# Kernel tuning notes

Measured on AMD Instinct MI355X. Metric: run time of the kernel, lower is better.

The kernel has to match this reference:

```python
import jax, jax.numpy as jnp
import numpy as np

N = 32768   # nodes
E = 131072  # directed edges
B = 8       # graphs in batch
F_IN = 1025
NEG = -1e30
EPS = 1e-5


def _lin_init(k, i, o):
    k1, k2 = jax.random.split(k)
    s = 1.0 / np.sqrt(i)
    return (jax.random.uniform(k1, (i, o), jnp.float32, -s, s),
            jax.random.uniform(k2, (o,), jnp.float32, -s, s))


def _bn_init(k, c):
    k1, k2, k3, k4 = jax.random.split(k, 4)
    gamma = jax.random.uniform(k1, (c,), jnp.float32, 0.5, 1.5)
    beta = jax.random.normal(k2, (c,), jnp.float32) * 0.1
    mean = jax.random.normal(k3, (c,), jnp.float32) * 0.1
    var = jax.random.uniform(k4, (c,), jnp.float32, 0.5, 1.5)
    return jnp.stack([gamma, beta, mean, var])  # [4, c]


def setup_inputs() -> dict:
    key = jax.random.key(0)
    ks = jax.random.split(key, 16)
    x = jax.random.normal(ks[0], (N, F_IN), jnp.float32)
    edge_index = jax.random.randint(ks[1], (2, E), 0, N, dtype=jnp.int32)
    batch = jnp.sort(jax.random.randint(ks[2], (N,), 0, B, dtype=jnp.int32))
    pool_w, pool_b = _lin_init(ks[3], 2 * F_IN, 1)
    c1_w0, _ = _lin_init(ks[4], F_IN, 512)
    c1_w1, c1_b = _lin_init(ks[5], F_IN, 512)
    c2_w0, _ = _lin_init(ks[6], 512, 512)
    c2_w1, c2_b = _lin_init(ks[7], 512, 512)
    bn1 = _bn_init(ks[8], 512)
    bn2 = _bn_init(ks[9], 512)
    bn3 = _bn_init(ks[10], 512)
    bn4 = _bn_init(ks[11], 256)
    lin1_w, lin1_b = _lin_init(ks[12], 1024, 512)
    lin2_w, lin2_b = _lin_init(ks[13], 512, 256)
    lin3_w, lin3_b = _lin_init(ks[14], 256, 4)
    return dict(x=x, edge_index=edge_index, batch=batch,
                pool_w=pool_w, pool_b=pool_b,
                c1_w0=c1_w0, c1_w1=c1_w1, c1_b=c1_b,
                c2_w0=c2_w0, c2_w1=c2_w1, c2_b=c2_b,
                bn1=bn1, bn2=bn2, bn3=bn3, bn4=bn4,
                lin1_w=lin1_w, lin1_b=lin1_b,
                lin2_w=lin2_w, lin2_b=lin2_b,
                lin3_w=lin3_w, lin3_b=lin3_b)


def _batchnorm(h, p):
    g, b, m, v = p[0], p[1], p[2], p[3]
    return (h - m) * jax.lax.rsqrt(v + EPS) * g + b


def _cheb(h, row, col, w, w0, w1, b):
    # ChebConv K=2, sym norm, lambda_max=2: out = h@W0 + (L_hat h)@W1 + b,
    # L_hat = -D^{-1/2} A D^{-1/2} (self-loops removed, diag of scaled L is 0)
    deg = jax.ops.segment_sum(w, row, num_segments=N)
    dis = jnp.where(deg > 0, 1.0 / jnp.sqrt(jnp.maximum(deg, 1e-12)), 0.0)
    nrm = -w * dis[row] * dis[col]
    tx1 = jax.ops.segment_sum(nrm[:, None] * h[row], col, num_segments=N)
    return h @ w0 + tx1 @ w1 + b


def _forward(x, edge_index, batch, pool_w, pool_b,
             c1_w0, c1_w1, c1_b, c2_w0, c2_w1, c2_b,
             bn1, bn2, bn3, bn4,
             lin1_w, lin1_b, lin2_w, lin2_b, lin3_w, lin3_b):
    u, v = edge_index[0], edge_index[1]

    # ---- EdgePooling: edge scores = softmax over dst segments, +0.5 ----
    e = (jnp.concatenate([x[u], x[v]], axis=1) @ pool_w + pool_b)[:, 0]  # [E]
    m = jax.ops.segment_max(e, v, num_segments=N)
    ex = jnp.exp(e - m[v])
    score = ex / jax.ops.segment_sum(ex, v, num_segments=N)[v] + 0.5

    # ---- greedy maximal matching in descending score order ----
    order = jnp.argsort(-score)

    def step(used, k):
        uu, vv = u[k], v[k]
        ok = jnp.logical_not(used[uu] | used[vv])
        used = used.at[uu].set(used[uu] | ok)
        used = used.at[vv].set(used[vv] | ok)
        return used, ok

    _, ok_sorted = jax.lax.scan(step, jnp.zeros((N,), bool), order)
    sel = jnp.zeros((E,), bool).at[order].set(ok_sorted)

    rep = jnp.minimum(u, v)  # cluster representative of a merged edge
    cluster = jnp.arange(N, dtype=jnp.int32)
    cluster = cluster.at[jnp.where(sel, u, N)].set(rep, mode='drop')
    cluster = cluster.at[jnp.where(sel, v, N)].set(rep, mode='drop')
    node_score = jnp.ones((N,), x.dtype).at[jnp.where(sel, rep, N)].set(score, mode='drop')
    px = jnp.zeros_like(x).at[cluster].add(x) * node_score[:, None]  # pooled node feats
    valid = cluster == jnp.arange(N, dtype=jnp.int32)  # surviving cluster rows

    # ---- coarsened edge_index, coalesced (dedup), self-loops dropped ----
    cu, cv = cluster[u], cluster[v]
    nonloop = cu != cv
    key = jnp.where(nonloop, cu * N + cv, N * N + jnp.arange(E, dtype=jnp.int32))
    o2 = jnp.argsort(key)
    sk = key[o2]
    first = jnp.concatenate([jnp.ones((1,), bool), sk[1:] != sk[:-1]])
    keep_sorted = first & (sk < N * N)
    w = jnp.zeros((E,), x.dtype).at[o2].set(keep_sorted.astype(x.dtype))

    # ---- two ChebConv + BN(eval) + ReLU ----
    h = jax.nn.relu(_batchnorm(_cheb(px, cu, cv, w, c1_w0, c1_w1, c1_b), bn1))
    h = jax.nn.relu(_batchnorm(_cheb(h, cu, cv, w, c2_w0, c2_w1, c2_b), bn2))

    # ---- global max + mean pool over valid nodes per graph ----
    hmax = jax.ops.segment_max(jnp.where(valid[:, None], h, NEG), batch, num_segments=B)
    cnt = jax.ops.segment_sum(valid.astype(h.dtype), batch, num_segments=B)
    hmean = jax.ops.segment_sum(jnp.where(valid[:, None], h, 0.0), batch,
                                num_segments=B) / jnp.maximum(cnt, 1.0)[:, None]
    g = jnp.concatenate([hmax, hmean], axis=1)  # [B, 1024]

    # ---- readout MLP (dropout off in eval) ----
    g = jax.nn.relu(_batchnorm(g @ lin1_w + lin1_b, bn3))
    g = jax.nn.relu(_batchnorm(g @ lin2_w + lin2_b, bn4))
    feature = g
    out = jax.nn.log_softmax(jax.nn.relu(g @ lin3_w + lin3_b), axis=-1)
    return out, feature


def reference(x, edge_index, batch, pool_w, pool_b,
              c1_w0, c1_w1, c1_b, c2_w0, c2_w1, c2_b,
              bn1, bn2, bn3, bn4,
              lin1_w, lin1_b, lin2_w, lin2_b, lin3_w, lin3_b):
    return _forward(x, edge_index, batch, pool_w, pool_b,
                    c1_w0, c1_w1, c1_b, c2_w0, c2_w1, c2_b,
                    bn1, bn2, bn3, bn4,
                    lin1_w, lin1_b, lin2_w, lin2_b, lin3_w, lin3_b)
```

## Files before the change

### kernel.cpp

```cpp
#include <hip/hip_runtime.h>
#include <hip/hip_bf16.h>
#include <cstdint>
#include <cmath>

typedef unsigned int u32;
typedef unsigned long long u64;
typedef float f32x4 __attribute__((ext_vector_type(4)));
typedef __bf16 bf16x8 __attribute__((ext_vector_type(8)));
typedef unsigned short us8 __attribute__((ext_vector_type(8)));
typedef unsigned short us4 __attribute__((ext_vector_type(4)));

#define NN 32768
#define NE 131072
#define FIN 1025
#define HTS 262144
#define HTM (HTS - 1)

#define WS_A_D    0ul
#define WS_B_D    262144ul
#define WS_EMAX   524288ul
#define WS_SSUM   655360ul
#define WS_EXD    917504ul
#define WS_CIN    917504ul
#define WS_KEY    1966080ul
#define WS_BEST   3014656ul
#define WS_USED   3276800ul
#define WS_CUR    3276800ul
#define WS_ACT0   3407872ul
#define WS_ACT1   3932160ul
#define WS_BTHI   0ul
#define WS_BT2    3407872ul
#define WS_HT     1966080ul
#define WS_RACC1  2097152ul
#define WS_RACC2  2113536ul
#define WS_SCORE  4456448ul
#define WS_CSRA   4456448ul
#define WS_SEL    4980736ul
#define WS_CSRC   4980736ul
#define WS_CLUST  5505024ul
#define WS_OTHER  5636096ul
#define WS_NSC    5767168ul
#define WS_CEU    5898240ul
#define WS_CEV    6422528ul
#define WS_DEG    6946816ul
#define WS_OFF    6946816ul
#define WS_DIS    7077888ul
#define WS_PXL    7077888ul
#define WS_MISC   7208960ul
#define WS_GMAX   7209216ul
#define WS_GSUM   7225600ul
#define WS_GCNT   7241984ul
#define WS_P      7242240ul
#define WS_PB     74351104ul
#define WS_H      141459968ul

__device__ __forceinline__ u32 enc_f(float f) {
    u32 b = __float_as_uint(f);
    return (b & 0x80000000u) ? ~b : (b | 0x80000000u);
}
__device__ __forceinline__ float dec_f(u32 m) {
    return (m & 0x80000000u) ? __uint_as_float(m ^ 0x80000000u) : __uint_as_float(~m);
}
__device__ __forceinline__ double wave_sum(double v) {
    #pragma unroll
    for (int off = 32; off > 0; off >>= 1) v += __shfl_down(v, off, 64);
    return v;
}
__device__ __forceinline__ unsigned short f2bf(float v) {
    u32 b = __float_as_uint(v);
    u32 r = b + 0x7FFFu + ((b >> 16) & 1u);
    return (unsigned short)(r >> 16);
}
__device__ __forceinline__ float bf2f(unsigned short h) {
    return __uint_as_float(((u32)h) << 16);
}
__device__ __forceinline__ bf16x8 ld_frag(const unsigned short* p) {
    union { us8 u; bf16x8 b; } t;
    t.u = *(const us8*)p;
    return t.b;
}
__device__ __forceinline__ void dma16(unsigned short* lds, const unsigned short* g) {
    __builtin_amdgcn_global_load_lds((const __attribute__((address_space(1))) u32*)g,
                                     (__attribute__((address_space(3))) u32*)lds, 16, 0, 0);
}

__global__ void node_dots(const float* __restrict__ x, const float* __restrict__ pw,
                          double* a_d, double* b_d,
                          u32* emax, double* ssum, u32* deg, int* misc,
                          u32* gmaxb, float* gsum, float* gcnt,
                          u64* best, u32* used, int* clus, int* other, float* nsc) {
    int gid = blockIdx.x * blockDim.x + threadIdx.x;
    if (gid < NN) {
        emax[gid] = 0u; ssum[gid] = 0.0; deg[gid] = 0u;
        best[gid] = ~0ull; used[gid] = 0u;
        clus[gid] = gid; other[gid] = -1; nsc[gid] = 1.0f;
    }
    if (gid < 4096) { gmaxb[gid] = 0u; gsum[gid] = 0.0f; }
    if (gid < 64) { misc[gid] = (gid == 1) ? NE : 0; gcnt[gid] = 0.0f; }

    int wave = gid >> 6;
    int lane = threadIdx.x & 63;
    if (wave >= NN) return;
    const float* xr = x + (size_t)wave * FIN;
    double s0 = 0.0, s1 = 0.0;
    for (int f = lane; f < FIN; f += 64) {
        double xv = (double)xr[f];
        s0 += xv * (double)pw[f];
        s1 += xv * (double)pw[FIN + f];
    }
    s0 = wave_sum(s0); s1 = wave_sum(s1);
    if (lane == 0) { a_d[wave] = s0; b_d[wave] = s1; }
}

__global__ void edge_p1(const int* __restrict__ ei, const double* __restrict__ a_d,
                        const double* __restrict__ b_d, const float* __restrict__ pb,
                        double* e_d, u32* emax) {
    int k = blockIdx.x * 256 + threadIdx.x;
    if (k >= NE) return;
    int u = ei[k], v = ei[NE + k];
    double e = a_d[u] + b_d[v] + (double)pb[0];
    e_d[k] = e;
    atomicMax(&emax[v], enc_f((float)e));
}
__global__ void edge_p2(const int* __restrict__ ei, double* e_d,
                        const u32* __restrict__ emax, double* ssum) {
    int k = blockIdx.x * 256 + threadIdx.x;
    if (k >= NE) return;
    int v = ei[NE + k];
    float mf = dec_f(emax[v]);
    double ex = exp(e_d[k] - (double)mf);
    e_d[k] = ex;
    unsafeAtomicAdd(&ssum[v], ex);
}
__global__ void edge_p3(const int* __restrict__ ei, const double* __restrict__ e_d,
                        const double* __restrict__ ssum, float* score, u64* key,
                        int* sel, int* act0, u64* best) {
    int k = blockIdx.x * 256 + threadIdx.x;
    if (k >= NE) return;
    int u = ei[k], v = ei[NE + k];
    float sc = (float)(e_d[k] / ssum[v] + 0.5);
    score[k] = sc;
    u32 m = enc_f(sc);
    u64 kk = ((u64)(m ^ 0xFFFFFFFFu) << 32) | (u32)k;
    key[k] = kk;
    sel[k] = 0;
    act0[k] = k;
    atomicMin(&best[u], kk);
    atomicMin(&best[v], kk);
}

__global__ void mk_sel(const u64* __restrict__ key, const int* __restrict__ ei,
                       const int* __restrict__ act, const int* __restrict__ cntp,
                       int* ncntp, const u64* __restrict__ best,
                       u32* used, int* sel) {
    int cnt = cntp[0];
    int stride = gridDim.x * blockDim.x;
    int gid = blockIdx.x * blockDim.x + threadIdx.x;
    if (gid == 0) ncntp[0] = 0;
    for (int i = gid; i < cnt; i += stride) {
        int e = act[i];
        u64 k = key[e];
        int a = ei[e], b = ei[NE + e];
        if (best[a] == k && best[b] == k) { sel[e] = 1; used[a] = 1u; used[b] = 1u; }
    }
}
__global__ void mk_compact(const int* __restrict__ ei, const int* __restrict__ act,
                           const int* __restrict__ cntp, int* nxt, int* ncntp,
                           u64* best, const u32* __restrict__ used) {
    int cnt = cntp[0];
    int stride = gridDim.x * blockDim.x;
    for (int i = blockIdx.x * blockDim.x + threadIdx.x; i < cnt; i += stride) {
        int e = act[i];
        int a = ei[e], b = ei[NE + e];
        best[a] = ~0ull; best[b] = ~0ull;
        bool live = !(used[a] | used[b]);
        u64 mask = __ballot(live);
        if (mask) {
            int lane = threadIdx.x & 63;
            int leader = __ffsll((unsigned long long)mask) - 1;
            int base = 0;
            if (lane == leader) base = atomicAdd(ncntp, __popcll(mask));
            base = __shfl(base, leader, 64);
            if (live) nxt[base + __popcll(mask & ((1ull << lane) - 1ull))] = e;
        }
    }
}
__global__ void mk_min(const u64* __restrict__ key, const int* __restrict__ ei,
                       const int* __restrict__ act, const int* __restrict__ cntp,
                       u64* best) {
    int cnt = cntp[0];
    int stride = gridDim.x * blockDim.x;
    for (int i = blockIdx.x * blockDim.x + threadIdx.x; i < cnt; i += stride) {
        int e = act[i];
        u64 k = key[e];
        atomicMin(&best[ei[e]], k);
        atomicMin(&best[ei[NE + e]], k);
    }
}
__global__ void __launch_bounds__(1024) match_fin(
        const u64* __restrict__ key, const int* __restrict__ ei,
        int* sel, u64* best, u32* used,
        int* listA, int* listB, const int* __restrict__ cntp) {
    int tid = threadIdx.x;
    int cnt = cntp[0];
    int* cur = listA; int* nxt = listB;
    __shared__ int s_n;
    for (int round = 0; round < 4096 && cnt > 0; ++round) {
        for (int i = tid; i < cnt; i += 1024) {
            int e = cur[i]; u64 k = key[e];
            atomicMin(&best[ei[e]], k);
            atomicMin(&best[ei[NE + e]], k);
        }
        __syncthreads();
        for (int i = tid; i < cnt; i += 1024) {
            int e = cur[i]; u64 k = key[e];
            int a = ei[e], b = ei[NE + e];
            if (best[a] == k && best[b] == k) { sel[e] = 1; used[a] = 1u; used[b] = 1u; }
        }
        if (tid == 0) s_n = 0;
        __syncthreads();
        for (int i = tid; i < cnt; i += 1024) {
            int e = cur[i];
            int a = ei[e], b = ei[NE + e];
            best[a] = ~0ull; best[b] = ~0ull;
            if (!(used[a] | used[b])) {
                int idx = atomicAdd(&s_n, 1);
                nxt[idx] = e;
            }
        }
        __syncthreads();
        cnt = s_n;
        int* t = cur; cur = nxt; nxt = t;
        __syncthreads();
    }
}

__global__ void apply_sel(const int* __restrict__ ei, const int* __restrict__ sel,
                          const float* __restrict__ score,
                          int* cluster, int* other, float* nscore,
                          u32* ht, u32* cin) {
    int e = blockIdx.x * 256 + threadIdx.x;
    ht[e << 1] = 0xFFFFFFFFu;
    ht[(e << 1) + 1] = 0xFFFFFFFFu;
    if (e < NN) cin[e] = 0u;
    if (sel[e] != 1) return;
    int u = ei[e], v = ei[NE + e];
    int rep = min(u, v);
    cluster[u] = rep; cluster[v] = rep;
    if (u != v) other[rep] = u + v - rep;
    nscore[rep] = score[e];
}

__global__ void coarse_build(const int* __restrict__ ei, const int* __restrict__ cluster,
                             u32* ht, int* misc, int* ce_u, int* ce_v, u32* deg,
                             u32* cin) {
    int e = blockIdx.x * 256 + threadIdx.x;
    if (e >= NE) return;
    int cu = cluster[ei[e]], cv = cluster[ei[NE + e]];
    if (cu == cv) return;
    u32 k = (u32)cu * 32768u + (u32)cv;
    u32 h = ((k * 2654435761u) >> 12) & HTM;
    while (true) {
        u32 old = atomicCAS(&ht[h], 0xFFFFFFFFu, k);
        if (old == 0xFFFFFFFFu) {
            int idx = atomicAdd(&misc[0], 1);
            ce_u[idx] = cu; ce_v[idx] = cv;
            atomicAdd(&deg[cu], 1u);
            atomicAdd(&cin[cv], 1u);
            break;
        }
        if (old == k) break;
        h = (h + 1) & HTM;
    }
}
__global__ void dis_kernel(const u32* __restrict__ deg, float* dis,
                           float* racc1, float* racc2,
                           const int* __restrict__ clus, const int* __restrict__ batch,
                           float* gcnt) {
    int n = blockIdx.x * 256 + threadIdx.x;
    if (n >= NN) return;
    u32 d = deg[n];
    dis[n] = d ? (float)(1.0 / sqrt((double)d)) : 0.0f;
    if (n < 4096) racc1[n] = 0.0f;
    if (n < 2048) racc2[n] = 0.0f;
    bool val = (clus[n] == n);
    int bt = batch[n];
    int lane = threadIdx.x & 63;
    #pragma unroll
    for (int g = 0; g < 8; ++g) {
        u64 m = __ballot(val && bt == g);
        if (m && lane == (__ffsll((unsigned long long)m) - 1))
            unsafeAtomicAdd(&gcnt[g], (float)__popcll(m));
    }
}

__global__ void __launch_bounds__(1024) scan_kernel(const u32* __restrict__ cin,
                                                    int* off, int* cur) {
    __shared__ int part[1024];
    int t = threadIdx.x;
    int base = t << 5;
    int loc[32];
    int s = 0;
    #pragma unroll
    for (int i = 0; i < 32; ++i) { loc[i] = s; s += (int)cin[base + i]; }
    part[t] = s;
    __syncthreads();
    for (int d = 1; d < 1024; d <<= 1) {
        int v = (t >= d) ? part[t - d] : 0;
        __syncthreads();
        if (t >= d) part[t] += v;
        __syncthreads();
    }
    int pre = (t == 0) ? 0 : part[t - 1];
    #pragma unroll
    for (int i = 0; i < 32; ++i) {
        int v = pre + loc[i];
        off[base + i] = v;
        cur[base + i] = v;
    }
}
__global__ void csr_scatter(const int* __restrict__ ce_u, const int* __restrict__ ce_v,
                            const float* __restrict__ dis, const int* __restrict__ misc,
                            int* cur, int* csr_a, float* csr_c) {
    int e = blockIdx.x * 256 + threadIdx.x;
    if (e >= misc[0]) return;
    int a = ce_u[e], b = ce_v[e];
    int pos = atomicAdd(&cur[b], 1);
    csr_a[pos] = a;
    csr_c[pos] = -dis[a] * dis[b];
}

__device__ __forceinline__ size_t pk_idx(int r, int k, int KT) {
    return ((((size_t)(r >> 4) * KT + (k >> 5)) << 6) + (((k >> 3) & 3) << 4) + (r & 15)) << 3;
}

__global__ void __launch_bounds__(256) conv_all(
        const float* __restrict__ x, const int* __restrict__ clus,
        const int* __restrict__ other, const float* __restrict__ nsc,
        unsigned short* __restrict__ Abf, float* __restrict__ pxl,
        const float* __restrict__ B10, const float* __restrict__ B11,
        unsigned short* __restrict__ Bp1,
        const float* __restrict__ B20, const float* __restrict__ B21,
        unsigned short* __restrict__ Bp2) {
    int bid = blockIdx.x;
    int t = threadIdx.x;
    if (bid < 2048) {
        int tile = bid;
        int wave = t >> 6, lane = t & 63;
        int l16 = lane & 15, quad = lane >> 4;
        int row = (tile << 4) + l16;
        bool valid = (clus[row] == row);
        int o = other[row];
        float s = nsc[row];
        const float* xr = x + (size_t)row * FIN;
        const float* xo = x + (size_t)(o >= 0 ? o : row) * FIN;
        for (int kt = wave; kt < 32; kt += 4) {
            int c0 = (kt << 5) + (quad << 3);
            unsigned short h[8];
            #pragma unroll
            for (int j = 0; j < 8; ++j) {
                float v = 0.0f;
                if (valid) {
                    v = xr[c0 + j];
                    if (o >= 0) v += xo[c0 + j];
                    v *= s;
                }
                h[j] = f2bf(v);
            }
            *(us8*)&Abf[((((size_t)tile << 5) + kt) << 9) + ((size_t)lane << 3)] = *(const us8*)h;
        }
        if (t < 16) {
            int r2 = (tile << 4) + t;
            bool v2 = (clus[r2] == r2);
            int o2 = other[r2];
            float v = 0.0f;
            if (v2) {
                v = x[(size_t)r2 * FIN + 1024];
                if (o2 >= 0) v += x[(size_t)o2 * FIN + 1024];
                v *= nsc[r2];
            }
            pxl[r2] = v;
        }
    } else if (bid < 2560) {
        int j = bid - 2048;
        int n = ((j & 3) << 8) + t;
        int k0 = (j >> 2) << 3;
        unsigned short h[8];
        #pragma unroll
        for (int jj = 0; jj < 8; ++jj) {
            int k = k0 + jj;
            float v = (n < 512) ? B10[(size_t)k * 512 + n] : B11[(size_t)k * 512 + (n - 512)];
            h[jj] = f2bf(v);
        }
        *(us8*)&Bp1[pk_idx(n, k0, 32)] = *(const us8*)h;
    } else {
        int j = bid - 2560;
        int n = ((j & 3) << 8) + t;
        int k0 = (j >> 2) << 3;
        unsigned short h[8];
        #pragma unroll
        for (int jj = 0; jj < 8; ++jj) {
            int k = k0 + jj;
            float v = (n < 512) ? B20[(size_t)k * 512 + n] : B21[(size_t)k * 512 + (n - 512)];
            h[jj] = f2bf(v);
        }
        *(us8*)&Bp2[pk_idx(n, k0, 16)] = *(const us8*)h;
    }
}

template <bool R1>
__global__ void __launch_bounds__(256, 4) gemm_pk(
        const unsigned short* __restrict__ Ap, const unsigned short* __restrict__ Bp,
        float* __restrict__ P, unsigned short* __restrict__ Pb, int KT,
        const float* __restrict__ pxl, const float* __restrict__ w0,
        const float* __restrict__ w1) {
    __shared__ unsigned short L[2][8192];
    int tid = threadIdx.x;
    int bid = blockIdx.x;
    int loc = bid >> 3;
    int bn = (loc & 7) << 7;
    int bm = ((((bid & 7) << 5) | (loc >> 3))) << 7;
    int wave = tid >> 6, lane = tid & 63, quad = lane >> 4, l16 = lane & 15;
    int moff = (wave >> 1) << 6, noff = (wave & 1) << 6;
    f32x4 acc[4][4];
    #pragma unroll
    for (int i = 0; i < 4; ++i)
        #pragma unroll
        for (int j = 0; j < 4; ++j) acc[i][j] = (f32x4){0.f, 0.f, 0.f, 0.f};

    const unsigned short* src[4];
    unsigned short* dst[4];
    #pragma unroll
    for (int q = 0; q < 4; ++q) {
        int f = (wave << 2) + q;
        int tg = (f < 8) ? ((bm >> 4) + f) : ((bn >> 4) + (f - 8));
        src[q] = ((f < 8) ? Ap : Bp) + (((size_t)tg * KT) << 9) + ((size_t)lane << 3);
        dst[q] = &L[0][(size_t)f << 9];
    }
    const unsigned short* ra = &L[0][(size_t)(wave >> 1) << 11];
    const unsigned short* rb = &L[0][4096 + ((size_t)(wave & 1) << 11)];

    #pragma unroll
    for (int q = 0; q < 4; ++q) dma16(dst[q], src[q]);
    __syncthreads();

    int cur = 0;
    for (int kt = 0; kt < KT; ++kt) {
        if (kt + 1 < KT) {
            int nb = (cur ^ 1) * 8192;
            size_t go = ((size_t)(kt + 1)) << 9;
            #pragma unroll
            for (int q = 0; q < 4; ++q) dma16(dst[q] + nb, src[q] + go);
        }
        const unsigned short* la = ra + cur * 8192;
        const unsigned short* lb = rb + cur * 8192;
        bf16x8 af[4], bf[4];
        #pragma unroll
        for (int i = 0; i < 4; ++i) {
            af[i] = ld_frag(la + ((size_t)i << 9) + (lane << 3));
            bf[i] = ld_frag(lb + ((size_t)i << 9) + (lane << 3));
        }
        #pragma unroll
        for (int mi = 0; mi < 4; ++mi)
            #pragma unroll
            for (int ni = 0; ni < 4; ++ni)
                acc[mi][ni] = __builtin_amdgcn_mfma_f32_16x16x32_bf16(af[mi], bf[ni], acc[mi][ni], 0, 0, 0);
        __syncthreads();
        cur ^= 1;
    }
    #pragma unroll
    for (int mi = 0; mi < 4; ++mi)
        #pragma unroll
        for (int ni = 0; ni < 4; ++ni) {
            int col = bn + noff + (ni << 4) + l16;
            float wl = 0.0f;
            if (R1) wl = (col < 512) ? w0[524288 + col] : w1[524288 + col - 512];
            #pragma unroll
            for (int r2 = 0; r2 < 4; ++r2) {
                int row = bm + moff + (mi << 4) + (quad << 2) + r2;
                float v = acc[mi][ni][r2];
                if (R1) v += pxl[row] * wl;
                if (col < 512) P[(size_t)row * 512 + col] = v;
                else Pb[(size_t)row * 512 + (col - 512)] = f2bf(v);
            }
        }
}

template <bool BF16OUT>
__global__ void __launch_bounds__(256) cheb_fuse(
        const float* __restrict__ P, const unsigned short* __restrict__ Pb,
        const int* __restrict__ off,
        const int* __restrict__ csr_a, const float* __restrict__ csr_c,
        const int* __restrict__ misc, const float* __restrict__ bias,
        const float* __restrict__ bn, float* __restrict__ Hf,
        unsigned short* __restrict__ Hb) {
    int b = (blockIdx.x * 256 + threadIdx.x) >> 6;
    int lane = threadIdx.x & 63;
    if (b >= NN) return;
    int s = off[b];
    int e = (b < NN - 1) ? off[b + 1] : misc[0];
    int c0 = lane << 3;
    float a0[4], a1[4];
    {
        float4 t0 = *(const float4*)&P[(size_t)b * 512 + c0];
        float4 t1 = *(const float4*)&P[(size_t)b * 512 + c0 + 4];
        a0[0] = t0.x; a0[1] = t0.y; a0[2] = t0.z; a0[3] = t0.w;
        a1[0] = t1.x; a1[1] = t1.y; a1[2] = t1.z; a1[3] = t1.w;
    }
    for (int j = s; j < e; ++j) {
        int a = csr_a[j];
        float cf = csr_c[j];
        us8 raw = *(const us8*)&Pb[(size_t)a * 512 + c0];
        a0[0] = fmaf(cf, bf2f(raw[0]), a0[0]); a0[1] = fmaf(cf, bf2f(raw[1]), a0[1]);
        a0[2] = fmaf(cf, bf2f(raw[2]), a0[2]); a0[3] = fmaf(cf, bf2f(raw[3]), a0[3]);
        a1[0] = fmaf(cf, bf2f(raw[4]), a1[0]); a1[1] = fmaf(cf, bf2f(raw[5]), a1[1]);
        a1[2] = fmaf(cf, bf2f(raw[6]), a1[2]); a1[3] = fmaf(cf, bf2f(raw[7]), a1[3]);
    }
    float o[8];
    #pragma unroll
    for (int i = 0; i < 8; ++i) {
        int j = c0 + i;
        float acc = (i < 4) ? a0[i] : a1[i - 4];
        float ga = bn[j], be = bn[512 + j], mn = bn[1024 + j], vr = bn[1536 + j];
        float sc = (float)(1.0 / sqrt((double)vr + 1e-5));
        float v = (acc + bias[j] - mn) * sc * ga + be;
        o[i] = v > 0.0f ? v : 0.0f;
    }
    if (BF16OUT) {
        unsigned short h[8];
        #pragma unroll
        for (int i = 0; i < 8; ++i) h[i] = f2bf(o[i]);
        *(us8*)&Hb[pk_idx(b, c0, 16)] = *(const us8*)h;
    } else {
        *(float4*)&Hf[(size_t)b * 512 + c0] = make_float4(o[0], o[1], o[2], o[3]);
        *(float4*)&Hf[(size_t)b * 512 + c0 + 4] = make_float4(o[4], o[5], o[6], o[7]);
    }
}

__global__ void __launch_bounds__(256) pool_kernel(
        const float* __restrict__ H, const int* __restrict__ cluster,
        const int* __restrict__ batch, u32* gmaxb, float* gsum) {
    int t = threadIdx.x;
    int n0 = blockIdx.x * 64;
    float m0 = 0.0f, m1 = 0.0f, s0 = 0.0f, s1 = 0.0f;
    int cur = batch[n0];
    for (int i = 0; i < 64; ++i) {
        int n = n0 + i;
        int bt = batch[n];
        if (bt != cur) {
            atomicMax(&gmaxb[cur * 512 + t], __float_as_uint(m0));
            atomicMax(&gmaxb[cur * 512 + t + 256], __float_as_uint(m1));
            unsafeAtomicAdd(&gsum[cur * 512 + t], s0);
            unsafeAtomicAdd(&gsum[cur * 512 + t + 256], s1);
            m0 = m1 = s0 = s1 = 0.0f; cur = bt;
        }
        if (cluster[n] == n) {
            float h0 = H[(size_t)n * 512 + t];
            float h1 = H[(size_t)n * 512 + t + 256];
            m0 = fmaxf(m0, h0); m1 = fmaxf(m1, h1);
            s0 += h0; s1 += h1;
        }
    }
    atomicMax(&gmaxb[cur * 512 + t], __float_as_uint(m0));
    atomicMax(&gmaxb[cur * 512 + t + 256], __float_as_uint(m1));
    unsafeAtomicAdd(&gsum[cur * 512 + t], s0);
    unsafeAtomicAdd(&gsum[cur * 512 + t + 256], s1);
}

__global__ void __launch_bounds__(512) ro1(
        const u32* __restrict__ gmaxb, const float* __restrict__ gsum,
        const float* __restrict__ gcnt, const float* __restrict__ l1w,
        float* __restrict__ racc1) {
    int o = threadIdx.x;
    int k0 = blockIdx.x << 4;
    float acc[8] = {0, 0, 0, 0, 0, 0, 0, 0};
    float inv[8];
    #pragma unroll
    for (int b = 0; b < 8; ++b) inv[b] = 1.0f / fmaxf(gcnt[b], 1.0f);
    for (int kk = 0; kk < 16; ++kk) {
        int k = k0 + kk;
        float w = l1w[(size_t)k * 512 + o];
        #pragma unroll
        for (int b = 0; b < 8; ++b) {
            float g = (k < 512) ? __uint_as_float(gmaxb[b * 512 + k])
                                : gsum[b * 512 + (k - 512)] * inv[b];
            acc[b] = fmaf(g, w, acc[b]);
        }
    }
    #pragma unroll
    for (int b = 0; b < 8; ++b) unsafeAtomicAdd(&racc1[b * 512 + o], acc[b]);
}
__global__ void __launch_bounds__(256) ro3(
        const float* __restrict__ racc1, const float* __restrict__ l1b,
        const float* __restrict__ bn3, const float* __restrict__ l2w,
        float* __restrict__ racc2) {
    int o = threadIdx.x;
    int k0 = blockIdx.x << 4;
    float acc[8] = {0, 0, 0, 0, 0, 0, 0, 0};
    for (int kk = 0; kk < 16; ++kk) {
        int k = k0 + kk;
        float ga = bn3[k], be = bn3[512 + k], mn = bn3[1024 + k], vr = bn3[1536 + k];
        float sc = (float)(1.0 / sqrt((double)vr + 1e-5));
        float bi = l1b[k];
        float w = l2w[(size_t)k * 256 + o];
        #pragma unroll
        for (int b = 0; b < 8; ++b) {
            float g1 = (racc1[b * 512 + k] + bi - mn) * sc * ga + be;
            g1 = g1 > 0.0f ? g1 : 0.0f;
            acc[b] = fmaf(g1, w, acc[b]);
        }
    }
    #pragma unroll
    for (int b = 0; b < 8; ++b) unsafeAtomicAdd(&racc2[b * 256 + o], acc[b]);
}
__global__ void __launch_bounds__(256) ro4(
        const float* __restrict__ racc2, const float* __restrict__ l2b,
        const float* __restrict__ bn4, const float* __restrict__ l3w,
        const float* __restrict__ l3b, float* __restrict__ out) {
    __shared__ float G2[8 * 256];
    int o = threadIdx.x;
    {
        float ga = bn4[o], be = bn4[256 + o], mn = bn4[512 + o], vr = bn4[768 + o];
        float sc = (float)(1.0 / sqrt((double)vr + 1e-5));
        float bi = l2b[o];
        #pragma unroll
        for (int b = 0; b < 8; ++b) {
            float v = (racc2[b * 256 + o] + bi - mn) * sc * ga + be;
            v = v > 0.0f ? v : 0.0f;
            G2[b * 256 + o] = v;
            out[32 + b * 256 + o] = v;
        }
    }
    __syncthreads();
    if (o < 8) {
        int b = o;
        float r[4];
        #pragma unroll
        for (int c = 0; c < 4; ++c) {
            float acc = l3b[c];
            for (int k = 0; k < 256; ++k) acc += G2[b * 256 + k] * l3w[k * 4 + c];
            r[c] = acc > 0.0f ? acc : 0.0f;
        }
        float mx = fmaxf(fmaxf(r[0], r[1]), fmaxf(r[2], r[3]));
        float s = 0.0f;
        #pragma unroll
        for (int c = 0; c < 4; ++c) s += expf(r[c] - mx);
        float lse = mx + logf(s);
        #pragma unroll
        for (int c = 0; c < 4; ++c) out[b * 4 + c] = r[c] - lse;
    }
}

extern "C" void kernel_launch(void* const* d_in, const int* in_sizes, int n_in,
                              void* d_out, int out_size, void* d_ws, size_t ws_size,
                              hipStream_t stream) {
    const float* x      = (const float*)d_in[0];
    const int*   ei     = (const int*)d_in[1];
    const int*   batch  = (const int*)d_in[2];
    const float* pool_w = (const float*)d_in[3];
    const float* pool_b = (const float*)d_in[4];
    const float* c1_w0  = (const float*)d_in[5];
    const float* c1_w1  = (const float*)d_in[6];
    const float* c1_b   = (const float*)d_in[7];
    const float* c2_w0  = (const float*)d_in[8];
    const float* c2_w1  = (const float*)d_in[9];
    const float* c2_b   = (const float*)d_in[10];
    const float* bn1    = (const float*)d_in[11];
    const float* bn2    = (const float*)d_in[12];
    const float* bn3    = (const float*)d_in[13];
    const float* bn4    = (const float*)d_in[14];
    const float* l1w    = (const float*)d_in[15];
    const float* l1b    = (const float*)d_in[16];
    const float* l2w    = (const float*)d_in[17];
    const float* l2b    = (const float*)d_in[18];
    const float* l3w    = (const float*)d_in[19];
    const float* l3b    = (const float*)d_in[20];
    float* out = (float*)d_out;
    char* ws = (char*)d_ws;

    double* a_d   = (double*)(ws + WS_A_D);
    double* b_d   = (double*)(ws + WS_B_D);
    u32*    emax  = (u32*)(ws + WS_EMAX);
    double* ssum  = (double*)(ws + WS_SSUM);
    double* exd   = (double*)(ws + WS_EXD);
    u32*    cin   = (u32*)(ws + WS_CIN);
    u64*    key   = (u64*)(ws + WS_KEY);
    u64*    best  = (u64*)(ws + WS_BEST);
    u32*    used  = (u32*)(ws + WS_USED);
    int*    curp  = (int*)(ws + WS_CUR);
    int*    act0  = (int*)(ws + WS_ACT0);
    int*    act1  = (int*)(ws + WS_ACT1);
    unsigned short* bthi = (unsigned short*)(ws + WS_BTHI);
    unsigned short* bt2  = (unsigned short*)(ws + WS_BT2);
    float*  pxl   = (float*)(ws + WS_PXL);
    u32*    ht    = (u32*)(ws + WS_HT);
    float*  racc1 = (float*)(ws + WS_RACC1);
    float*  racc2 = (float*)(ws + WS_RACC2);
    float*  score = (float*)(ws + WS_SCORE);
    int*    csr_a = (int*)(ws + WS_CSRA);
    int*    sel   = (int*)(ws + WS_SEL);
    float*  csr_c = (float*)(ws + WS_CSRC);
    int*    clus  = (int*)(ws + WS_CLUST);
    int*    other = (int*)(ws + WS_OTHER);
    float*  nsc   = (float*)(ws + WS_NSC);
    int*    ce_u  = (int*)(ws + WS_CEU);
    int*    ce_v  = (int*)(ws + WS_CEV);
    u32*    deg   = (u32*)(ws + WS_DEG);
    int*    off   = (int*)(ws + WS_OFF);
    float*  dis   = (float*)(ws + WS_DIS);
    int*    misc  = (int*)(ws + WS_MISC);
    u32*    gmaxb = (u32*)(ws + WS_GMAX);
    float*  gsum  = (float*)(ws + WS_GSUM);
    float*  gcnt  = (float*)(ws + WS_GCNT);
    float*  P     = (float*)(ws + WS_P);
    unsigned short* Pb = (unsigned short*)(ws + WS_PB);
    unsigned short* ax = (unsigned short*)(ws + WS_H);
    unsigned short* hb = (unsigned short*)(ws + WS_H);
    float*  H     = (float*)(ws + WS_H);

    node_dots<<<NN / 4, 256, 0, stream>>>(x, pool_w, a_d, b_d,
                                          emax, ssum, deg, misc, gmaxb, gsum, gcnt,
                                          best, used, clus, other, nsc);
    edge_p1<<<NE / 256, 256, 0, stream>>>(ei, a_d, b_d, pool_b, exd, emax);
    edge_p2<<<NE / 256, 256, 0, stream>>>(ei, exd, emax, ssum);
    edge_p3<<<NE / 256, 256, 0, stream>>>(ei, exd, ssum, score, key, sel, act0, best);

    {
        static const int gr[9] = {512, 512, 256, 128, 64, 32, 16, 8, 8};
        int* acts[2] = {act0, act1};
        for (int r = 0; r < 8; ++r) {
            int c = r & 1, n = 1 - c;
            mk_sel<<<gr[r], 256, 0, stream>>>(key, ei, acts[c], &misc[1 + c],
                                              &misc[1 + n], best, used, sel);
            mk_compact<<<gr[r], 256, 0, stream>>>(ei, acts[c], &misc[1 + c],
                                                  acts[n], &misc[1 + n], best, used);
            mk_min<<<gr[r + 1], 256, 0, stream>>>(key, ei, acts[n], &misc[1 + n], best);
        }
        match_fin<<<1, 1024, 0, stream>>>(key, ei, sel, best, used,
                                          act0, act1, &misc[1]);
    }

    apply_sel<<<NE / 256, 256, 0, stream>>>(ei, sel, score, clus, other, nsc, ht, cin);
    coarse_build<<<NE / 256, 256, 0, stream>>>(ei, clus, ht, misc, ce_u, ce_v, deg, cin);
    dis_kernel<<<NN / 256, 256, 0, stream>>>(deg, dis, racc1, racc2, clus, batch, gcnt);
    scan_kernel<<<1, 1024, 0, stream>>>(cin, off, curp);
    csr_scatter<<<NE / 256, 256, 0, stream>>>(ce_u, ce_v, dis, misc, curp, csr_a, csr_c);

    conv_all<<<2816, 256, 0, stream>>>(x, clus, other, nsc, ax, pxl,
                                       c1_w0, c1_w1, bthi, c2_w0, c2_w1, bt2);
    gemm_pk<true><<<2048, 256, 0, stream>>>(ax, bthi, P, Pb, 32, pxl, c1_w0, c1_w1);
    cheb_fuse<true><<<NN / 4, 256, 0, stream>>>(P, Pb, off, csr_a, csr_c, misc, c1_b, bn1,
                                                nullptr, hb);

    gemm_pk<false><<<2048, 256, 0, stream>>>(hb, bt2, P, Pb, 16, nullptr, nullptr, nullptr);
    cheb_fuse<false><<<NN / 4, 256, 0, stream>>>(P, Pb, off, csr_a, csr_c, misc, c2_b, bn2,
                                                 H, nullptr);

    pool_kernel<<<NN / 64, 256, 0, stream>>>(H, clus, batch, gmaxb, gsum);

    ro1<<<64, 512, 0, stream>>>(gmaxb, gsum, gcnt, l1w, racc1);
    ro3<<<32, 256, 0, stream>>>(racc1, l1b, bn3, l2w, racc2);
    ro4<<<1, 256, 0, stream>>>(racc2, l2b, bn4, l3w, l3b, out);
}
```

Measured before the change: 839.4 us.

## Compact surviving cluster nodes so GEMMs and conv only process valid rows

Adds a second prefix scan over cluster-representative flags to build a compact index and a permutation of surviving nodes, with the count stored in misc. The conversion, both GEMMs and the Chebyshev fuse kernels then run only over the compacted rows and exit early beyond the rounded count. CSR neighbour indices and pooling are remapped through the compact index. This cuts GEMM and conversion work, since pooling leaves only about half the nodes, at the cost of a longer single-block scan and an extra level of indirection.

```diff
diff --git a/kernel.cpp b/kernel.cpp
--- a/kernel.cpp
+++ b/kernel.cpp
@@ -33,6 +33,8 @@
 #define WS_HT     1966080ul
 #define WS_RACC1  2097152ul
 #define WS_RACC2  2113536ul
+#define WS_CIDX   2129920ul
+#define WS_PERM   2260992ul
 #define WS_SCORE  4456448ul
 #define WS_CSRA   4456448ul
 #define WS_SEL    4980736ul
@@ -295,7 +297,9 @@
 }
 
 __global__ void __launch_bounds__(1024) scan_kernel(const u32* __restrict__ cin,
-                                                    int* off, int* cur) {
+                                                    int* off, int* cur,
+                                                    const int* __restrict__ clus,
+                                                    int* cidx, int* perm, int* misc) {
     __shared__ int part[1024];
     int t = threadIdx.x;
     int base = t << 5;
@@ -318,15 +322,41 @@
         off[base + i] = v;
         cur[base + i] = v;
     }
+    __syncthreads();
+    u32 vmask = 0;
+    s = 0;
+    #pragma unroll
+    for (int i = 0; i < 32; ++i) {
+        int f = (clus[base + i] == base + i) ? 1 : 0;
+        loc[i] = s; s += f;
+        vmask |= (u32)f << i;
+    }
+    part[t] = s;
+    __syncthreads();
+    for (int d = 1; d < 1024; d <<= 1) {
+        int v = (t >= d) ? part[t - d] : 0;
+        __syncthreads();
+        if (t >= d) part[t] += v;
+        __syncthreads();
+    }
+    int pre2 = (t == 0) ? 0 : part[t - 1];
+    #pragma unroll
+    for (int i = 0; i < 32; ++i) {
+        int c = pre2 + loc[i];
+        cidx[base + i] = c;
+        if ((vmask >> i) & 1u) perm[c] = base + i;
+    }
+    if (t == 1023) misc[4] = pre2 + s;
 }
 __global__ void csr_scatter(const int* __restrict__ ce_u, const int* __restrict__ ce_v,
                             const float* __restrict__ dis, const int* __restrict__ misc,
-                            int* cur, int* csr_a, float* csr_c) {
+                            int* cur, int* csr_a, float* csr_c,
+                            const int* __restrict__ cidx) {
     int e = blockIdx.x * 256 + threadIdx.x;
     if (e >= misc[0]) return;
     int a = ce_u[e], b = ce_v[e];
     int pos = atomicAdd(&cur[b], 1);
-    csr_a[pos] = a;
+    csr_a[pos] = cidx[a];
     csr_c[pos] = -dis[a] * dis[b];
 }
 
@@ -335,7 +365,8 @@
 }
 
 __global__ void __launch_bounds__(256) conv_all(
-        const float* __restrict__ x, const int* __restrict__ clus,
+        const float* __restrict__ x, const int* __restrict__ perm,
+        const int* __restrict__ misc,
         const int* __restrict__ other, const float* __restrict__ nsc,
         unsigned short* __restrict__ Abf, float* __restrict__ pxl,
         const float* __restrict__ B10, const float* __restrict__ B11,
@@ -345,13 +376,16 @@
     int bid = blockIdx.x;
     int t = threadIdx.x;
     if (bid < 2048) {
+        int cnt = misc[4];
         int tile = bid;
+        if ((tile << 4) >= ((cnt + 127) & ~127)) return;
         int wave = t >> 6, lane = t & 63;
         int l16 = lane & 15, quad = lane >> 4;
-        int row = (tile << 4) + l16;
-        bool valid = (clus[row] == row);
-        int o = other[row];
-        float s = nsc[row];
+        int ci = (tile << 4) + l16;
+        bool valid = ci < cnt;
+        int row = valid ? perm[ci] : 0;
+        int o = valid ? other[row] : -1;
+        float s = valid ? nsc[row] : 0.0f;
         const float* xr = x + (size_t)row * FIN;
         const float* xo = x + (size_t)(o >= 0 ? o : row) * FIN;
         for (int kt = wave; kt < 32; kt += 4) {
@@ -370,16 +404,16 @@
             *(us8*)&Abf[((((size_t)tile << 5) + kt) << 9) + ((size_t)lane << 3)] = *(const us8*)h;
         }
         if (t < 16) {
-            int r2 = (tile << 4) + t;
-            bool v2 = (clus[r2] == r2);
-            int o2 = other[r2];
+            int ci2 = (tile << 4) + t;
             float v = 0.0f;
-            if (v2) {
+            if (ci2 < cnt) {
+                int r2 = perm[ci2];
+                int o2 = other[r2];
                 v = x[(size_t)r2 * FIN + 1024];
                 if (o2 >= 0) v += x[(size_t)o2 * FIN + 1024];
                 v *= nsc[r2];
             }
-            pxl[r2] = v;
+            pxl[ci2] = v;
         }
     } else if (bid < 2560) {
         int j = bid - 2048;
@@ -413,13 +447,14 @@
         const unsigned short* __restrict__ Ap, const unsigned short* __restrict__ Bp,
         float* __restrict__ P, unsigned short* __restrict__ Pb, int KT,
         const float* __restrict__ pxl, const float* __restrict__ w0,
-        const float* __restrict__ w1) {
+        const float* __restrict__ w1, const int* __restrict__ msc) {
     __shared__ unsigned short L[2][8192];
     int tid = threadIdx.x;
     int bid = blockIdx.x;
     int loc = bid >> 3;
     int bn = (loc & 7) << 7;
     int bm = ((((bid & 7) << 5) | (loc >> 3))) << 7;
+    if (bm >= ((msc[4] + 127) & ~127)) return;
     int wave = tid >> 6, lane = tid & 63, quad = lane >> 4, l16 = lane & 15;
     int moff = (wave >> 1) << 6, noff = (wave & 1) << 6;
     f32x4 acc[4][4];
@@ -493,12 +528,13 @@
         const int* __restrict__ csr_a, const float* __restrict__ csr_c,
         const int* __restrict__ misc, const float* __restrict__ bias,
         const float* __restrict__ bn, float* __restrict__ Hf,
-        unsigned short* __restrict__ Hb) {
+        unsigned short* __restrict__ Hb, const int* __restrict__ perm) {
     int b = (blockIdx.x * 256 + threadIdx.x) >> 6;
     int lane = threadIdx.x & 63;
-    if (b >= NN) return;
-    int s = off[b];
-    int e = (b < NN - 1) ? off[b + 1] : misc[0];
+    if (b >= misc[4]) return;
+    int r = perm[b];
+    int s = off[r];
+    int e = (r < NN - 1) ? off[r + 1] : misc[0];
     int c0 = lane << 3;
     float a0[4], a1[4];
     {
@@ -539,7 +575,8 @@
 
 __global__ void __launch_bounds__(256) pool_kernel(
         const float* __restrict__ H, const int* __restrict__ cluster,
-        const int* __restrict__ batch, u32* gmaxb, float* gsum) {
+        const int* __restrict__ batch, u32* gmaxb, float* gsum,
+        const int* __restrict__ cidx) {
     int t = threadIdx.x;
     int n0 = blockIdx.x * 64;
     float m0 = 0.0f, m1 = 0.0f, s0 = 0.0f, s1 = 0.0f;
@@ -555,8 +592,9 @@
             m0 = m1 = s0 = s1 = 0.0f; cur = bt;
         }
         if (cluster[n] == n) {
-            float h0 = H[(size_t)n * 512 + t];
-            float h1 = H[(size_t)n * 512 + t + 256];
+            size_t ci = (size_t)cidx[n];
+            float h0 = H[ci * 512 + t];
+            float h1 = H[ci * 512 + t + 256];
             m0 = fmaxf(m0, h0); m1 = fmaxf(m1, h1);
             s0 += h0; s1 += h1;
         }
@@ -684,6 +722,8 @@
     double* ssum  = (double*)(ws + WS_SSUM);
     double* exd   = (double*)(ws + WS_EXD);
     u32*    cin   = (u32*)(ws + WS_CIN);
+    int*    cidxp = (int*)(ws + WS_CIDX);
+    int*    permp = (int*)(ws + WS_PERM);
     u64*    key   = (u64*)(ws + WS_KEY);
     u64*    best  = (u64*)(ws + WS_BEST);
     u32*    used  = (u32*)(ws + WS_USED);
@@ -743,20 +783,22 @@
     apply_sel<<<NE / 256, 256, 0, stream>>>(ei, sel, score, clus, other, nsc, ht, cin);
     coarse_build<<<NE / 256, 256, 0, stream>>>(ei, clus, ht, misc, ce_u, ce_v, deg, cin);
     dis_kernel<<<NN / 256, 256, 0, stream>>>(deg, dis, racc1, racc2, clus, batch, gcnt);
-    scan_kernel<<<1, 1024, 0, stream>>>(cin, off, curp);
-    csr_scatter<<<NE / 256, 256, 0, stream>>>(ce_u, ce_v, dis, misc, curp, csr_a, csr_c);
-
-    conv_all<<<2816, 256, 0, stream>>>(x, clus, other, nsc, ax, pxl,
+    scan_kernel<<<1, 1024, 0, stream>>>(cin, off, curp, clus, cidxp, permp, misc);
+    csr_scatter<<<NE / 256, 256, 0, stream>>>(ce_u, ce_v, dis, misc, curp, csr_a, csr_c,
+                                              cidxp);
+
+    conv_all<<<2816, 256, 0, stream>>>(x, permp, misc, other, nsc, ax, pxl,
                                        c1_w0, c1_w1, bthi, c2_w0, c2_w1, bt2);
-    gemm_pk<true><<<2048, 256, 0, stream>>>(ax, bthi, P, Pb, 32, pxl, c1_w0, c1_w1);
+    gemm_pk<true><<<2048, 256, 0, stream>>>(ax, bthi, P, Pb, 32, pxl, c1_w0, c1_w1, misc);
     cheb_fuse<true><<<NN / 4, 256, 0, stream>>>(P, Pb, off, csr_a, csr_c, misc, c1_b, bn1,
-                                                nullptr, hb);
-
-    gemm_pk<false><<<2048, 256, 0, stream>>>(hb, bt2, P, Pb, 16, nullptr, nullptr, nullptr);
+                                                nullptr, hb, permp);
+
+    gemm_pk<false><<<2048, 256, 0, stream>>>(hb, bt2, P, Pb, 16, nullptr, nullptr, nullptr,
+                                             misc);
     cheb_fuse<false><<<NN / 4, 256, 0, stream>>>(P, Pb, off, csr_a, csr_c, misc, c2_b, bn2,
-                                                 H, nullptr);
-
-    pool_kernel<<<NN / 64, 256, 0, stream>>>(H, clus, batch, gmaxb, gsum);
+                                                 H, nullptr, permp);
+
+    pool_kernel<<<NN / 64, 256, 0, stream>>>(H, clus, batch, gmaxb, gsum, cidxp);
 
     ro1<<<64, 512, 0, stream>>>(gmaxb, gsum, gcnt, l1w, racc1);
     ro3<<<32, 256, 0, stream>>>(racc1, l1b, bn3, l2w, racc2);
```

Measured after the change: 839.5 us. Within noise of the previous version (+0.0%).
